# Kernel tuning notes

Measured on AMD Instinct MI355X. Metric: run time of the kernel, lower is better.

The kernel has to match this reference:

```python
import jax, jax.numpy as jnp
import numpy as np

N0, N1, N2, N3 = 100000, 25000, 6250, 1600
DEG = 16
D_IN, D_H = 512, 256


def setup_inputs() -> dict:
    key = jax.random.key(0)
    ks = jax.random.split(key, 20)
    inp = {}
    inp["x"] = jax.random.normal(ks[0], (N0, D_IN), dtype=jnp.float32)
    # bipartite blocks: (src_ids into previous frontier, dst_ids into next frontier)
    inp["src0"] = jax.random.randint(ks[1], (N1 * DEG,), 0, N0)
    inp["dst0"] = jax.random.randint(ks[2], (N1 * DEG,), 0, N1)
    inp["src1"] = jax.random.randint(ks[3], (N2 * DEG,), 0, N1)
    inp["dst1"] = jax.random.randint(ks[4], (N2 * DEG,), 0, N2)
    inp["src2"] = jax.random.randint(ks[5], (N3 * DEG,), 0, N2)
    inp["dst2"] = jax.random.randint(ks[6], (N3 * DEG,), 0, N3)
    def xavier(k, shp):
        fan_in, fan_out = shp
        lim = jnp.sqrt(6.0 / (fan_in + fan_out))
        return jax.random.uniform(k, shp, jnp.float32, -lim, lim)
    inp["Ws0"] = xavier(ks[7], (D_IN, D_H)); inp["Wn0"] = xavier(ks[8], (D_IN, D_H)); inp["b0"] = jnp.zeros((D_H,), jnp.float32)
    inp["Ws1"] = xavier(ks[9], (D_H, D_H)); inp["Wn1"] = xavier(ks[10], (D_H, D_H)); inp["b1"] = jnp.zeros((D_H,), jnp.float32)
    inp["Ws2"] = xavier(ks[11], (D_H, D_H)); inp["Wn2"] = xavier(ks[12], (D_H, D_H)); inp["b2"] = jnp.zeros((D_H,), jnp.float32)
    inp["W_fc"] = xavier(ks[13], (D_H, D_H)); inp["b_fc"] = jnp.zeros((D_H,), jnp.float32)
    return inp


def _sage_mean(h, src, dst, n_dst, Ws, Wn, b):
    # DGL SAGEConv('mean') on a bipartite block: out = h_dst@Ws + mean_neigh@Wn + b
    h_dst = h[:n_dst]                                   # [n_dst, d]
    msg = h[src]                                        # [E, d] gather
    agg = jax.ops.segment_sum(msg, dst, num_segments=n_dst)
    deg = jax.ops.segment_sum(jnp.ones(src.shape, h.dtype), dst, num_segments=n_dst)
    mean = agg / jnp.maximum(deg, 1.0)[:, None]
    return h_dst @ Ws + mean @ Wn + b


def reference(x, src0, dst0, src1, dst1, src2, dst2,
              Ws0, Wn0, b0, Ws1, Wn1, b1, Ws2, Wn2, b2, W_fc, b_fc):
    h = _sage_mean(x, src0, dst0, N1, Ws0, Wn0, b0)
    h = jax.nn.relu(h)  # dropout is identity in eval mode
    h = _sage_mean(h, src1, dst1, N2, Ws1, Wn1, b1)
    h = jax.nn.relu(h)
    h = _sage_mean(h, src2, dst2, N3, Ws2, Wn2, b2)
    return h @ W_fc + b_fc
```

## Files before the change

kernel.cpp:

```cpp
#include <hip/hip_runtime.h>
#include <hip/hip_bf16.h>
#include <cstddef>
#include <cstdint>

#define N0 100000
#define N1 25000
#define N2 6250
#define N3 1600
#define DEG 16
#define D_IN 512
#define D_H 256

#define E0 (N1*DEG)
#define E1 (N2*DEG)
#define E2 (N3*DEG)

typedef _Float16 half_t;
typedef __attribute__((ext_vector_type(8))) _Float16 f16x8;
typedef __attribute__((ext_vector_type(4))) _Float16 f16x4;
typedef __attribute__((ext_vector_type(4))) float f32x4;

__global__ void hist3_kernel(const int* __restrict__ d0, const int* __restrict__ d1,
                             const int* __restrict__ d2,
                             int* __restrict__ c0, int* __restrict__ c1, int* __restrict__ c2)
{
    const int i = blockIdx.x * 256 + threadIdx.x;
    if (i < E0)            atomicAdd(&c0[d0[i]], 1);
    else if (i < E0 + E1)  atomicAdd(&c1[d1[i - E0]], 1);
    else if (i < E0 + E1 + E2) atomicAdd(&c2[d2[i - E0 - E1]], 1);
}

__global__ void fill3_kernel(const int* __restrict__ s0, const int* __restrict__ d0,
                             const int* __restrict__ s1, const int* __restrict__ d1,
                             const int* __restrict__ s2, const int* __restrict__ d2,
                             int* __restrict__ u0, int* __restrict__ u1, int* __restrict__ u2,
                             int* __restrict__ e0, int* __restrict__ e1, int* __restrict__ e2)
{
    const int i = blockIdx.x * 256 + threadIdx.x;
    if (i < E0) {
        const int p = atomicAdd(&u0[d0[i]], 1); e0[p] = s0[i];
    } else if (i < E0 + E1) {
        const int j = i - E0;
        const int p = atomicAdd(&u1[d1[j]], 1); e1[p] = s1[j];
    } else if (i < E0 + E1 + E2) {
        const int j = i - E0 - E1;
        const int p = atomicAdd(&u2[d2[j]], 1); e2[p] = s2[j];
    }
}

__global__ __launch_bounds__(1024)
void scan3_kernel(const int* __restrict__ c0, int* __restrict__ p0, int* __restrict__ u0,
                  const int* __restrict__ c1, int* __restrict__ p1, int* __restrict__ u1,
                  const int* __restrict__ c2, int* __restrict__ p2, int* __restrict__ u2)
{
    const int b = blockIdx.x;
    const int* cnt = (b == 0) ? c0 : (b == 1) ? c1 : c2;
    int* ptr = (b == 0) ? p0 : (b == 1) ? p1 : p2;
    int* cur = (b == 0) ? u0 : (b == 1) ? u1 : u2;
    const int n = (b == 0) ? N1 : (b == 1) ? N2 : N3;

    const int t = threadIdx.x;
    const int chunk = (n + 1023) >> 10;
    const int beg = t * chunk;
    const int end = min(n, beg + chunk);

    int sum = 0;
    for (int i = beg; i < end; ++i) sum += cnt[i];

    const int lane = t & 63, wid = t >> 6;
    int inc = sum;
    #pragma unroll
    for (int d = 1; d < 64; d <<= 1) {
        int u = __shfl_up(inc, d, 64);
        if (lane >= d) inc += u;
    }
    __shared__ int wtot[16];
    __shared__ int total_s;
    if (lane == 63) wtot[wid] = inc;
    __syncthreads();
    if (wid == 0) {
        int w = (lane < 16) ? wtot[lane] : 0;
        int ws = w;
        #pragma unroll
        for (int d = 1; d < 16; d <<= 1) {
            int u = __shfl_up(ws, d, 64);
            if (lane >= d) ws += u;
        }
        if (lane < 16) wtot[lane] = ws - w;
        if (lane == 15) total_s = ws;
    }
    __syncthreads();
    int run = (inc - sum) + wtot[wid];
    for (int i = beg; i < end; ++i) {
        ptr[i] = run; cur[i] = run;
        run += cnt[i];
    }
    if (t == 0) ptr[n] = total_s;
}

__global__ __launch_bounds__(256)
void xconv_kernel(const float* __restrict__ x, half_t* __restrict__ xh, int n8)
{
    const int id = blockIdx.x * 256 + threadIdx.x;
    if (id >= n8) return;
    const float4* p = reinterpret_cast<const float4*>(x) + (size_t)id * 2;
    const float4 a = p[0], b = p[1];
    f16x8 o;
    o[0] = (half_t)a.x; o[1] = (half_t)a.y; o[2] = (half_t)a.z; o[3] = (half_t)a.w;
    o[4] = (half_t)b.x; o[5] = (half_t)b.y; o[6] = (half_t)b.z; o[7] = (half_t)b.w;
    *(reinterpret_cast<f16x8*>(xh) + id) = o;
}

__global__ __launch_bounds__(256)
void wconv_kernel(const float* s0, const float* s1, const float* s2, const float* s3,
                  const float* s4, const float* s5, const float* s6,
                  half_t* t0, half_t* t1, half_t* t2, half_t* t3,
                  half_t* t4, half_t* t5, half_t* t6)
{
    const int id = blockIdx.x * 256 + threadIdx.x;
    const float* src; half_t* dst; int kb; int e;
    if (id < 131072)      { src = s0; dst = t0; kb = 9; e = id; }
    else if (id < 262144) { src = s1; dst = t1; kb = 9; e = id - 131072; }
    else if (id < 327680) { src = s2; dst = t2; kb = 8; e = id - 262144; }
    else if (id < 393216) { src = s3; dst = t3; kb = 8; e = id - 327680; }
    else if (id < 458752) { src = s4; dst = t4; kb = 8; e = id - 393216; }
    else if (id < 524288) { src = s5; dst = t5; kb = 8; e = id - 458752; }
    else if (id < 589824) { src = s6; dst = t6; kb = 8; e = id - 524288; }
    else return;
    const int K = 1 << kb;
    const int nn = e >> kb, k = e & (K - 1);
    dst[((size_t)nn << kb) + k] = (half_t)src[(size_t)k * 256 + nn];
}

template<int K>
__global__ __launch_bounds__(256)
void csr_mean_f16(const half_t* __restrict__ h, const int* __restrict__ esrc,
                  const int* __restrict__ ptr, half_t* __restrict__ mean, int n)
{
    constexpr int TPN = K / 8;
    constexpr int NPB = 256 / TPN;
    const int node = blockIdx.x * NPB + threadIdx.x / TPN;
    const int lane = threadIdx.x % TPN;
    if (node >= n) return;
    const int beg = ptr[node], end = ptr[node + 1];
    float acc[8] = {};
    for (int p = beg; p < end; ++p) {
        const int s = esrc[p];
        const f16x8 v = *reinterpret_cast<const f16x8*>(h + (size_t)s * K + (size_t)lane * 8);
        #pragma unroll
        for (int i = 0; i < 8; ++i) acc[i] += (float)v[i];
    }
    const float r = 1.0f / fmaxf((float)(end - beg), 1.0f);
    f16x8 o;
    #pragma unroll
    for (int i = 0; i < 8; ++i) o[i] = (half_t)(acc[i] * r);
    *reinterpret_cast<f16x8*>(mean + (size_t)node * K + (size_t)lane * 8) = o;
}

#define GBM 64
#define GBK 32
#define LPAD 40

template<bool HAS_MEAN, bool RELU, bool OUT_F16>
__global__ __launch_bounds__(256)
void mfma_gemm(const half_t* __restrict__ A,
               const half_t* __restrict__ Mn,
               const half_t* __restrict__ WsT,
               const half_t* __restrict__ WnT,
               const float* __restrict__ bias,
               void* __restrict__ Cout,
               int M, int K)
{
    __shared__ half_t sA[GBM][LPAD];
    __shared__ half_t sB[256][LPAD];

    const int tid  = threadIdx.x;
    const int wid  = tid >> 6;
    const int lane = tid & 63;
    const int bm   = blockIdx.x * GBM;

    f32x4 acc[4][4] = {};

    const int npass = HAS_MEAN ? 2 : 1;
    for (int pass = 0; pass < npass; ++pass) {
        const half_t* __restrict__ Ap = pass ? Mn : A;
        const half_t* __restrict__ Wp = pass ? WnT : WsT;

        for (int k0 = 0; k0 < K; k0 += GBK) {
            {
                const int row = tid >> 2;
                const int kq  = (tid & 3) * 8;
                f16x8 v = {};
                if (bm + row < M)
                    v = *reinterpret_cast<const f16x8*>(Ap + (size_t)(bm + row) * K + k0 + kq);
                *reinterpret_cast<f16x8*>(&sA[row][kq]) = v;
            }
            {
                const int kq = (tid & 3) * 8;
                const int r0 = tid >> 2;
                #pragma unroll
                for (int j = 0; j < 4; ++j) {
                    const int row = r0 + 64 * j;
                    const f16x8 v = *reinterpret_cast<const f16x8*>(Wp + (size_t)row * K + k0 + kq);
                    *reinterpret_cast<f16x8*>(&sB[row][kq]) = v;
                }
            }
            __syncthreads();

            const int lrow = lane & 15;
            const int koff = (lane >> 4) * 8;
            f16x8 af[4], bf[4];
            #pragma unroll
            for (int m = 0; m < 4; ++m)
                af[m] = *reinterpret_cast<const f16x8*>(&sA[m * 16 + lrow][koff]);
            #pragma unroll
            for (int n = 0; n < 4; ++n)
                bf[n] = *reinterpret_cast<const f16x8*>(&sB[wid * 64 + n * 16 + lrow][koff]);
            #pragma unroll
            for (int m = 0; m < 4; ++m)
                #pragma unroll
                for (int n = 0; n < 4; ++n)
                    acc[m][n] = __builtin_amdgcn_mfma_f32_16x16x32_f16(af[m], bf[n], acc[m][n], 0, 0, 0);
            __syncthreads();
        }
    }

    const int lcol = lane & 15;
    const int rgrp = lane >> 4;
    #pragma unroll
    for (int m = 0; m < 4; ++m) {
        #pragma unroll
        for (int n = 0; n < 4; ++n) {
            const int col = wid * 64 + n * 16 + lcol;
            const float bv = bias[col];
            #pragma unroll
            for (int r = 0; r < 4; ++r) {
                const int row = bm + m * 16 + rgrp * 4 + r;
                if (row >= M) continue;
                float v = acc[m][n][r] + bv;
                if (RELU) v = fmaxf(v, 0.0f);
                if (OUT_F16) ((half_t*)Cout)[(size_t)row * 256 + col] = (half_t)v;
                else         ((float*)Cout)[(size_t)row * 256 + col] = v;
            }
        }
    }
}

static constexpr size_t align256(size_t x) { return (x + 255) & ~(size_t)255; }

extern "C" void kernel_launch(void* const* d_in, const int* in_sizes, int n_in,
                              void* d_out, int out_size, void* d_ws, size_t ws_size,
                              hipStream_t stream)
{
    const float* x    = (const float*)d_in[0];
    const int*  src0  = (const int*)d_in[1];
    const int*  dst0  = (const int*)d_in[2];
    const int*  src1  = (const int*)d_in[3];
    const int*  dst1  = (const int*)d_in[4];
    const int*  src2  = (const int*)d_in[5];
    const int*  dst2  = (const int*)d_in[6];
    const float* Ws0  = (const float*)d_in[7];
    const float* Wn0  = (const float*)d_in[8];
    const float* b0   = (const float*)d_in[9];
    const float* Ws1  = (const float*)d_in[10];
    const float* Wn1  = (const float*)d_in[11];
    const float* b1   = (const float*)d_in[12];
    const float* Ws2  = (const float*)d_in[13];
    const float* Wn2  = (const float*)d_in[14];
    const float* b2   = (const float*)d_in[15];
    const float* W_fc = (const float*)d_in[16];
    const float* b_fc = (const float*)d_in[17];
    float* out = (float*)d_out;

    char* ws = (char*)d_ws;
    size_t off = 0;
    const size_t cntA_off = off; off = align256(off + (size_t)(N1 + N2 + N3) * 4);
    const size_t ptr0_off = off; off = align256(off + (size_t)(N1 + 1) * 4);
    const size_t ptr1_off = off; off = align256(off + (size_t)(N2 + 1) * 4);
    const size_t ptr2_off = off; off = align256(off + (size_t)(N3 + 1) * 4);
    const size_t cur0_off = off; off = align256(off + (size_t)N1 * 4);
    const size_t cur1_off = off; off = align256(off + (size_t)N2 * 4);
    const size_t cur2_off = off; off = align256(off + (size_t)N3 * 4);
    const size_t es0_off  = off; off = align256(off + (size_t)E0 * 4);
    const size_t es1_off  = off; off = align256(off + (size_t)E1 * 4);
    const size_t es2_off  = off; off = align256(off + (size_t)E2 * 4);
    const size_t xh_off   = off; off = align256(off + (size_t)N0 * D_IN * 2);
    const size_t mean_off = off; off = align256(off + (size_t)N1 * D_IN * 2);
    const size_t h0_off   = off; off = align256(off + (size_t)N1 * D_H * 2);
    const size_t h1_off   = off; off = align256(off + (size_t)N2 * D_H * 2);
    const size_t h2_off   = off; off = align256(off + (size_t)N3 * D_H * 2);
    const size_t wt0_off  = off; off = align256(off + (size_t)D_IN * D_H * 2);
    const size_t wt1_off  = off; off = align256(off + (size_t)D_IN * D_H * 2);
    const size_t wt2_off  = off; off = align256(off + (size_t)D_H * D_H * 2);
    const size_t wt3_off  = off; off = align256(off + (size_t)D_H * D_H * 2);
    const size_t wt4_off  = off; off = align256(off + (size_t)D_H * D_H * 2);
    const size_t wt5_off  = off; off = align256(off + (size_t)D_H * D_H * 2);
    const size_t wt6_off  = off; off = align256(off + (size_t)D_H * D_H * 2);

    int* cnt0 = (int*)(ws + cntA_off);
    int* cnt1 = cnt0 + N1;
    int* cnt2 = cnt1 + N2;
    int* ptr0 = (int*)(ws + ptr0_off);
    int* ptr1 = (int*)(ws + ptr1_off);
    int* ptr2 = (int*)(ws + ptr2_off);
    int* cur0 = (int*)(ws + cur0_off);
    int* cur1 = (int*)(ws + cur1_off);
    int* cur2 = (int*)(ws + cur2_off);
    int* es0  = (int*)(ws + es0_off);
    int* es1  = (int*)(ws + es1_off);
    int* es2  = (int*)(ws + es2_off);
    half_t* xh   = (half_t*)(ws + xh_off);
    half_t* mean = (half_t*)(ws + mean_off);
    half_t* h0   = (half_t*)(ws + h0_off);
    half_t* h1   = (half_t*)(ws + h1_off);
    half_t* h2   = (half_t*)(ws + h2_off);
    half_t* WsT0 = (half_t*)(ws + wt0_off);
    half_t* WnT0 = (half_t*)(ws + wt1_off);
    half_t* WsT1 = (half_t*)(ws + wt2_off);
    half_t* WnT1 = (half_t*)(ws + wt3_off);
    half_t* WsT2 = (half_t*)(ws + wt4_off);
    half_t* WnT2 = (half_t*)(ws + wt5_off);
    half_t* WfcT = (half_t*)(ws + wt6_off);

    hipMemsetAsync(cnt0, 0, (size_t)(N1 + N2 + N3) * 4, stream);
    {
        const int tot = E0 + E1 + E2;
        hist3_kernel<<<(tot + 255) / 256, 256, 0, stream>>>(dst0, dst1, dst2, cnt0, cnt1, cnt2);
        scan3_kernel<<<3, 1024, 0, stream>>>(cnt0, ptr0, cur0, cnt1, ptr1, cur1, cnt2, ptr2, cur2);
        fill3_kernel<<<(tot + 255) / 256, 256, 0, stream>>>(
            src0, dst0, src1, dst1, src2, dst2, cur0, cur1, cur2, es0, es1, es2);
    }
    wconv_kernel<<<2304, 256, 0, stream>>>(Ws0, Wn0, Ws1, Wn1, Ws2, Wn2, W_fc,
                                           WsT0, WnT0, WsT1, WnT1, WsT2, WnT2, WfcT);
    {
        const int n8 = N0 * D_IN / 8;
        xconv_kernel<<<(n8 + 255) / 256, 256, 0, stream>>>(x, xh, n8);
    }

    {
        constexpr int NPB = 256 / (D_IN / 8);
        csr_mean_f16<D_IN><<<(N1 + NPB - 1) / NPB, 256, 0, stream>>>(xh, es0, ptr0, mean, N1);
        mfma_gemm<true, true, true><<<(N1 + GBM - 1) / GBM, 256, 0, stream>>>(
            xh, mean, WsT0, WnT0, b0, h0, N1, D_IN);
    }
    {
        constexpr int NPB = 256 / (D_H / 8);
        csr_mean_f16<D_H><<<(N2 + NPB - 1) / NPB, 256, 0, stream>>>(h0, es1, ptr1, mean, N2);
        mfma_gemm<true, true, true><<<(N2 + GBM - 1) / GBM, 256, 0, stream>>>(
            h0, mean, WsT1, WnT1, b1, h1, N2, D_H);
    }
    {
        constexpr int NPB = 256 / (D_H / 8);
        csr_mean_f16<D_H><<<(N3 + NPB - 1) / NPB, 256, 0, stream>>>(h1, es2, ptr2, mean, N3);
        mfma_gemm<true, false, true><<<(N3 + GBM - 1) / GBM, 256, 0, stream>>>(
            h1, mean, WsT2, WnT2, b2, h2, N3, D_H);
    }
    mfma_gemm<false, false, false><<<(N3 + GBM - 1) / GBM, 256, 0, stream>>>(
        h2, nullptr, WfcT, nullptr, b_fc, out, N3, D_H);
}
```

Measured before the change: 347.6 us.

## Fuse preprocessing kernels, batch neighbor index loads, use 8-wave GEMM blocks

Merges the x conversion, weight transpose/conversion and degree histogram into one launch to cut launch overhead and let the independent work overlap. The CSR mean kernel now loads up to TPN neighbor indices cooperatively, broadcasts them with shuffles and issues four gathers at a time for more memory-level parallelism. The GEMM moves to 512 threads per block, with each wave owning 32 output columns instead of 64, which lowers accumulator register pressure per wave at the cost of more waves sharing the same shared-memory tiles.

```diff
diff --git a/kernel.cpp b/kernel.cpp
--- a/kernel.cpp
+++ b/kernel.cpp
@@ -17,17 +17,51 @@
 
 typedef _Float16 half_t;
 typedef __attribute__((ext_vector_type(8))) _Float16 f16x8;
-typedef __attribute__((ext_vector_type(4))) _Float16 f16x4;
 typedef __attribute__((ext_vector_type(4))) float f32x4;
 
-__global__ void hist3_kernel(const int* __restrict__ d0, const int* __restrict__ d1,
-                             const int* __restrict__ d2,
-                             int* __restrict__ c0, int* __restrict__ c1, int* __restrict__ c2)
-{
-    const int i = blockIdx.x * 256 + threadIdx.x;
-    if (i < E0)            atomicAdd(&c0[d0[i]], 1);
-    else if (i < E0 + E1)  atomicAdd(&c1[d1[i - E0]], 1);
-    else if (i < E0 + E1 + E2) atomicAdd(&c2[d2[i - E0 - E1]], 1);
+#define XB 25000
+#define WB 2304
+#define HB (((E0+E1+E2) + 255) / 256)
+
+__global__ __launch_bounds__(256)
+void mega_conv_kernel(const float* __restrict__ x, half_t* __restrict__ xh,
+                      const float* s0, const float* s1, const float* s2, const float* s3,
+                      const float* s4, const float* s5, const float* s6,
+                      half_t* t0, half_t* t1, half_t* t2, half_t* t3,
+                      half_t* t4, half_t* t5, half_t* t6,
+                      const int* __restrict__ d0, const int* __restrict__ d1,
+                      const int* __restrict__ d2,
+                      int* __restrict__ c0, int* __restrict__ c1, int* __restrict__ c2)
+{
+    const int bid = blockIdx.x;
+    if (bid < XB) {
+        const int id = bid * 256 + threadIdx.x;
+        const float4* p = reinterpret_cast<const float4*>(x) + (size_t)id * 2;
+        const float4 a = p[0], b = p[1];
+        f16x8 o;
+        o[0] = (half_t)a.x; o[1] = (half_t)a.y; o[2] = (half_t)a.z; o[3] = (half_t)a.w;
+        o[4] = (half_t)b.x; o[5] = (half_t)b.y; o[6] = (half_t)b.z; o[7] = (half_t)b.w;
+        *(reinterpret_cast<f16x8*>(xh) + id) = o;
+    } else if (bid < XB + WB) {
+        const int id = (bid - XB) * 256 + threadIdx.x;
+        const float* src; half_t* dst; int kb; int e;
+        if (id < 131072)      { src = s0; dst = t0; kb = 9; e = id; }
+        else if (id < 262144) { src = s1; dst = t1; kb = 9; e = id - 131072; }
+        else if (id < 327680) { src = s2; dst = t2; kb = 8; e = id - 262144; }
+        else if (id < 393216) { src = s3; dst = t3; kb = 8; e = id - 327680; }
+        else if (id < 458752) { src = s4; dst = t4; kb = 8; e = id - 393216; }
+        else if (id < 524288) { src = s5; dst = t5; kb = 8; e = id - 458752; }
+        else if (id < 589824) { src = s6; dst = t6; kb = 8; e = id - 524288; }
+        else return;
+        const int K = 1 << kb;
+        const int nn = e >> kb, k = e & (K - 1);
+        dst[((size_t)nn << kb) + k] = (half_t)src[(size_t)k * 256 + nn];
+    } else {
+        const int i = (bid - XB - WB) * 256 + threadIdx.x;
+        if (i < E0)                atomicAdd(&c0[d0[i]], 1);
+        else if (i < E0 + E1)      atomicAdd(&c1[d1[i - E0]], 1);
+        else if (i < E0 + E1 + E2) atomicAdd(&c2[d2[i - E0 - E1]], 1);
+    }
 }
 
 __global__ void fill3_kernel(const int* __restrict__ s0, const int* __restrict__ d0,
@@ -98,40 +132,6 @@
     if (t == 0) ptr[n] = total_s;
 }
 
-__global__ __launch_bounds__(256)
-void xconv_kernel(const float* __restrict__ x, half_t* __restrict__ xh, int n8)
-{
-    const int id = blockIdx.x * 256 + threadIdx.x;
-    if (id >= n8) return;
-    const float4* p = reinterpret_cast<const float4*>(x) + (size_t)id * 2;
-    const float4 a = p[0], b = p[1];
-    f16x8 o;
-    o[0] = (half_t)a.x; o[1] = (half_t)a.y; o[2] = (half_t)a.z; o[3] = (half_t)a.w;
-    o[4] = (half_t)b.x; o[5] = (half_t)b.y; o[6] = (half_t)b.z; o[7] = (half_t)b.w;
-    *(reinterpret_cast<f16x8*>(xh) + id) = o;
-}
-
-__global__ __launch_bounds__(256)
-void wconv_kernel(const float* s0, const float* s1, const float* s2, const float* s3,
-                  const float* s4, const float* s5, const float* s6,
-                  half_t* t0, half_t* t1, half_t* t2, half_t* t3,
-                  half_t* t4, half_t* t5, half_t* t6)
-{
-    const int id = blockIdx.x * 256 + threadIdx.x;
-    const float* src; half_t* dst; int kb; int e;
-    if (id < 131072)      { src = s0; dst = t0; kb = 9; e = id; }
-    else if (id < 262144) { src = s1; dst = t1; kb = 9; e = id - 131072; }
-    else if (id < 327680) { src = s2; dst = t2; kb = 8; e = id - 262144; }
-    else if (id < 393216) { src = s3; dst = t3; kb = 8; e = id - 327680; }
-    else if (id < 458752) { src = s4; dst = t4; kb = 8; e = id - 393216; }
-    else if (id < 524288) { src = s5; dst = t5; kb = 8; e = id - 458752; }
-    else if (id < 589824) { src = s6; dst = t6; kb = 8; e = id - 524288; }
-    else return;
-    const int K = 1 << kb;
-    const int nn = e >> kb, k = e & (K - 1);
-    dst[((size_t)nn << kb) + k] = (half_t)src[(size_t)k * 256 + nn];
-}
-
 template<int K>
 __global__ __launch_bounds__(256)
 void csr_mean_f16(const half_t* __restrict__ h, const int* __restrict__ esrc,
@@ -144,11 +144,35 @@
     if (node >= n) return;
     const int beg = ptr[node], end = ptr[node + 1];
     float acc[8] = {};
-    for (int p = beg; p < end; ++p) {
-        const int s = esrc[p];
-        const f16x8 v = *reinterpret_cast<const f16x8*>(h + (size_t)s * K + (size_t)lane * 8);
-        #pragma unroll
-        for (int i = 0; i < 8; ++i) acc[i] += (float)v[i];
+    for (int base = beg; base < end; base += TPN) {
+        const int rem = end - base;
+        const int cnt = (rem < TPN) ? rem : TPN;
+        const int myidx = (lane < cnt) ? esrc[base + lane] : 0;
+        int j = 0;
+        for (; j + 3 < cnt; j += 4) {
+            const int a0 = __shfl(myidx, j + 0, TPN);
+            const int a1 = __shfl(myidx, j + 1, TPN);
+            const int a2 = __shfl(myidx, j + 2, TPN);
+            const int a3 = __shfl(myidx, j + 3, TPN);
+            const f16x8 v0 = *reinterpret_cast<const f16x8*>(h + (size_t)a0 * K + (size_t)lane * 8);
+            const f16x8 v1 = *reinterpret_cast<const f16x8*>(h + (size_t)a1 * K + (size_t)lane * 8);
+            const f16x8 v2 = *reinterpret_cast<const f16x8*>(h + (size_t)a2 * K + (size_t)lane * 8);
+            const f16x8 v3 = *reinterpret_cast<const f16x8*>(h + (size_t)a3 * K + (size_t)lane * 8);
+            #pragma unroll
+            for (int i = 0; i < 8; ++i) acc[i] += (float)v0[i];
+            #pragma unroll
+            for (int i = 0; i < 8; ++i) acc[i] += (float)v1[i];
+            #pragma unroll
+            for (int i = 0; i < 8; ++i) acc[i] += (float)v2[i];
+            #pragma unroll
+            for (int i = 0; i < 8; ++i) acc[i] += (float)v3[i];
+        }
+        for (; j < cnt; ++j) {
+            const int a0 = __shfl(myidx, j, TPN);
+            const f16x8 v0 = *reinterpret_cast<const f16x8*>(h + (size_t)a0 * K + (size_t)lane * 8);
+            #pragma unroll
+            for (int i = 0; i < 8; ++i) acc[i] += (float)v0[i];
+        }
     }
     const float r = 1.0f / fmaxf((float)(end - beg), 1.0f);
     f16x8 o;
@@ -162,7 +186,7 @@
 #define LPAD 40
 
 template<bool HAS_MEAN, bool RELU, bool OUT_F16>
-__global__ __launch_bounds__(256)
+__global__ __launch_bounds__(512)
 void mfma_gemm(const half_t* __restrict__ A,
                const half_t* __restrict__ Mn,
                const half_t* __restrict__ WsT,
@@ -179,7 +203,7 @@
     const int lane = tid & 63;
     const int bm   = blockIdx.x * GBM;
 
-    f32x4 acc[4][4] = {};
+    f32x4 acc[4][2] = {};
 
     const int npass = HAS_MEAN ? 2 : 1;
     for (int pass = 0; pass < npass; ++pass) {
@@ -187,7 +211,7 @@
         const half_t* __restrict__ Wp = pass ? WnT : WsT;
 
         for (int k0 = 0; k0 < K; k0 += GBK) {
-            {
+            if (tid < 256) {
                 const int row = tid >> 2;
                 const int kq  = (tid & 3) * 8;
                 f16x8 v = {};
@@ -199,8 +223,8 @@
                 const int kq = (tid & 3) * 8;
                 const int r0 = tid >> 2;
                 #pragma unroll
-                for (int j = 0; j < 4; ++j) {
-                    const int row = r0 + 64 * j;
+                for (int j = 0; j < 2; ++j) {
+                    const int row = r0 + 128 * j;
                     const f16x8 v = *reinterpret_cast<const f16x8*>(Wp + (size_t)row * K + k0 + kq);
                     *reinterpret_cast<f16x8*>(&sB[row][kq]) = v;
                 }
@@ -209,17 +233,17 @@
 
             const int lrow = lane & 15;
             const int koff = (lane >> 4) * 8;
-            f16x8 af[4], bf[4];
+            f16x8 af[4], bf[2];
             #pragma unroll
             for (int m = 0; m < 4; ++m)
                 af[m] = *reinterpret_cast<const f16x8*>(&sA[m * 16 + lrow][koff]);
             #pragma unroll
-            for (int n = 0; n < 4; ++n)
-                bf[n] = *reinterpret_cast<const f16x8*>(&sB[wid * 64 + n * 16 + lrow][koff]);
+            for (int n = 0; n < 2; ++n)
+                bf[n] = *reinterpret_cast<const f16x8*>(&sB[wid * 32 + n * 16 + lrow][koff]);
             #pragma unroll
             for (int m = 0; m < 4; ++m)
                 #pragma unroll
-                for (int n = 0; n < 4; ++n)
+                for (int n = 0; n < 2; ++n)
                     acc[m][n] = __builtin_amdgcn_mfma_f32_16x16x32_f16(af[m], bf[n], acc[m][n], 0, 0, 0);
             __syncthreads();
         }
@@ -230,8 +254,8 @@
     #pragma unroll
     for (int m = 0; m < 4; ++m) {
         #pragma unroll
-        for (int n = 0; n < 4; ++n) {
-            const int col = wid * 64 + n * 16 + lcol;
+        for (int n = 0; n < 2; ++n) {
+            const int col = wid * 32 + n * 16 + lcol;
             const float bv = bias[col];
             #pragma unroll
             for (int r = 0; r < 4; ++r) {
@@ -323,38 +347,36 @@
     half_t* WfcT = (half_t*)(ws + wt6_off);
 
     hipMemsetAsync(cnt0, 0, (size_t)(N1 + N2 + N3) * 4, stream);
+    mega_conv_kernel<<<XB + WB + HB, 256, 0, stream>>>(
+        x, xh,
+        Ws0, Wn0, Ws1, Wn1, Ws2, Wn2, W_fc,
+        WsT0, WnT0, WsT1, WnT1, WsT2, WnT2, WfcT,
+        dst0, dst1, dst2, cnt0, cnt1, cnt2);
+    scan3_kernel<<<3, 1024, 0, stream>>>(cnt0, ptr0, cur0, cnt1, ptr1, cur1, cnt2, ptr2, cur2);
     {
         const int tot = E0 + E1 + E2;
-        hist3_kernel<<<(tot + 255) / 256, 256, 0, stream>>>(dst0, dst1, dst2, cnt0, cnt1, cnt2);
-        scan3_kernel<<<3, 1024, 0, stream>>>(cnt0, ptr0, cur0, cnt1, ptr1, cur1, cnt2, ptr2, cur2);
         fill3_kernel<<<(tot + 255) / 256, 256, 0, stream>>>(
             src0, dst0, src1, dst1, src2, dst2, cur0, cur1, cur2, es0, es1, es2);
-    }
-    wconv_kernel<<<2304, 256, 0, stream>>>(Ws0, Wn0, Ws1, Wn1, Ws2, Wn2, W_fc,
-                                           WsT0, WnT0, WsT1, WnT1, WsT2, WnT2, WfcT);
-    {
-        const int n8 = N0 * D_IN / 8;
-        xconv_kernel<<<(n8 + 255) / 256, 256, 0, stream>>>(x, xh, n8);
     }
 
     {
         constexpr int NPB = 256 / (D_IN / 8);
         csr_mean_f16<D_IN><<<(N1 + NPB - 1) / NPB, 256, 0, stream>>>(xh, es0, ptr0, mean, N1);
-        mfma_gemm<true, true, true><<<(N1 + GBM - 1) / GBM, 256, 0, stream>>>(
+        mfma_gemm<true, true, true><<<(N1 + GBM - 1) / GBM, 512, 0, stream>>>(
             xh, mean, WsT0, WnT0, b0, h0, N1, D_IN);
     }
     {
         constexpr int NPB = 256 / (D_H / 8);
         csr_mean_f16<D_H><<<(N2 + NPB - 1) / NPB, 256, 0, stream>>>(h0, es1, ptr1, mean, N2);
-        mfma_gemm<true, true, true><<<(N2 + GBM - 1) / GBM, 256, 0, stream>>>(
+        mfma_gemm<true, true, true><<<(N2 + GBM - 1) / GBM, 512, 0, stream>>>(
             h0, mean, WsT1, WnT1, b1, h1, N2, D_H);
     }
     {
         constexpr int NPB = 256 / (D_H / 8);
         csr_mean_f16<D_H><<<(N3 + NPB - 1) / NPB, 256, 0, stream>>>(h1, es2, ptr2, mean, N3);
-        mfma_gemm<true, false, true><<<(N3 + GBM - 1) / GBM, 256, 0, stream>>>(
+        mfma_gemm<true, false, true><<<(N3 + GBM - 1) / GBM, 512, 0, stream>>>(
             h1, mean, WsT2, WnT2, b2, h2, N3, D_H);
     }
-    mfma_gemm<false, false, false><<<(N3 + GBM - 1) / GBM, 256, 0, stream>>>(
+    mfma_gemm<false, false, false><<<(N3 + GBM - 1) / GBM, 512, 0, stream>>>(
         h2, nullptr, WfcT, nullptr, b_fc, out, N3, D_H);
 }
```

Result: faster. 309.1 us (-11.1%).
